# Kernel optimization log

Measured on AMD Instinct MI355X. Metric: run time of the kernel, lower is better.

The kernel has to match this reference:

```python
import jax, jax.numpy as jnp
import numpy as np

B, T, D, H = 4, 2048, 1024, 16
DK = D // H


def setup_inputs() -> dict:
    key = jax.random.key(0)
    ks = jax.random.split(key, 8)
    s = 0.02
    return {
        "query": jax.random.normal(ks[0], (B, T, D), jnp.float32),
        "key": jax.random.normal(ks[1], (B, T, D), jnp.float32),
        "value": jax.random.normal(ks[2], (B, T, D), jnp.float32),
        "mask": jnp.ones((B, T, T), jnp.int32),  # 1 = attend, 0 = masked out
        "Wq": jax.random.normal(ks[3], (D, D), jnp.float32) * s,
        "bq": jnp.zeros((D,), jnp.float32),
        "Wk": jax.random.normal(ks[4], (D, D), jnp.float32) * s,
        "bk": jnp.zeros((D,), jnp.float32),
        "Wv": jax.random.normal(ks[5], (D, D), jnp.float32) * s,
        "bv": jnp.zeros((D,), jnp.float32),
        "Wo": jax.random.normal(ks[6], (D, D), jnp.float32) * s,
        "bo": jnp.zeros((D,), jnp.float32),
    }


def reference(query, key, value, mask, Wq, bq, Wk, bk, Wv, bv, Wo, bo):
    b, t1, d = query.shape
    h, dk = H, DK
    # linear projections (torch nn.Linear: x @ W.T + b), split heads
    q = (query @ Wq.T + bq).reshape(b, t1, h, dk).transpose(0, 2, 1, 3)  # b h t1 dk
    k = (key @ Wk.T + bk).reshape(b, -1, h, dk).transpose(0, 2, 1, 3)    # b h t2 dk
    v = (value @ Wv.T + bv).reshape(b, -1, h, dk).transpose(0, 2, 1, 3)  # b h t2 dk
    scores = jnp.einsum('bhqd,bhkd->bhqk', q, k) / jnp.sqrt(jnp.float32(dk))
    neg = jnp.finfo(scores.dtype).min
    m = (mask[:, None, :, :] == 0)  # b 1 t1 t2 broadcast over heads
    scores = jnp.where(m, neg, scores)
    attn = jax.nn.softmax(scores, axis=-1)
    attn = jnp.where(m, 0.0, attn)
    # dropout_rate = 0.0 -> identity
    x = jnp.einsum('bhqk,bhkd->bhqd', attn, v)
    x = x.transpose(0, 2, 1, 3).reshape(b, t1, h * dk)
    out = x @ Wo.T + bo
    return out, attn
```

## Files before the change

### kernel.cpp

```cpp
#include <hip/hip_runtime.h>
#include <hip/hip_bf16.h>
#include <stdint.h>

#define B_ 4
#define T_ 2048
#define D_ 1024
#define H_ 16
#define DK_ 64
#define LOG2E 1.44269504088896340736f
#define NEGF (-3.0e38f)

typedef __attribute__((ext_vector_type(8))) short bf16x8;
typedef __attribute__((ext_vector_type(4))) float f32x4;

#define FENCE()   asm volatile("" ::: "memory")
#define SCHEDB()  __builtin_amdgcn_sched_barrier(0)
#define SBAR()    __builtin_amdgcn_s_barrier()
#define WAITV0()  asm volatile("s_waitcnt vmcnt(0)" ::: "memory")
#define WAITL0()  asm volatile("s_waitcnt lgkmcnt(0)" ::: "memory")
#define WAITLV4() asm volatile("s_waitcnt lgkmcnt(0) vmcnt(4)" ::: "memory")

__device__ inline unsigned short f2bf(float f){
  union { __hip_bfloat16 h; unsigned short u; } v;
  v.h = __hip_bfloat16(f);
  return v.u;
}
__device__ inline unsigned int pk2(float a, float b){
  return (unsigned int)f2bf(a) | ((unsigned int)f2bf(b) << 16);
}
__device__ inline float fexp2(float x){ return __builtin_amdgcn_exp2f(x); }
__device__ inline f32x4 mfma16(bf16x8 a, bf16x8 b, f32x4 c){
  return __builtin_amdgcn_mfma_f32_16x16x32_bf16(a, b, c, 0, 0, 0);
}
__device__ inline bf16x8 lds_frag(const unsigned short* base, int row, int slot){
  return *(const bf16x8*)((const char*)base + row*128 + ((slot ^ (row & 7)) << 4));
}
__device__ inline void gload16(const void* g, void* l){
  __builtin_amdgcn_global_load_lds((const __attribute__((address_space(1))) void*)g,
                                   (__attribute__((address_space(3))) void*)l, 16, 0, 0);
}
__device__ inline void stage_gl128(const unsigned short* __restrict__ g, int ld,
                                   unsigned short* lds, int wave, int lane){
#pragma unroll
  for (int i = 0; i < 4; ++i){
    int row = wave*32 + i*8 + (lane >> 3);
    int c = (lane & 7) ^ (row & 7);
    gload16(g + (size_t)row*ld + c*8, lds + (wave*32 + i*8)*64);
  }
}
__device__ inline void stage_gl64(const unsigned short* __restrict__ g, int ld,
                                  unsigned short* lds, int wave, int lane){
#pragma unroll
  for (int i = 0; i < 2; ++i){
    int row = wave*16 + i*8 + (lane >> 3);
    int c = (lane & 7) ^ (row & 7);
    gload16(g + (size_t)row*ld + c*8, lds + (wave*16 + i*8)*64);
  }
}

__global__ void pack_mask_k(const int* __restrict__ mask, unsigned long long* __restrict__ bits){
  int i = blockIdx.x * 256 + threadIdx.x;
  unsigned long long b = __ballot(mask[i] != 0);
  if ((threadIdx.x & 63) == 0) bits[i >> 6] = b;
}

__global__ void convall_k(const float* __restrict__ Wq, const float* __restrict__ Wk,
                          const float* __restrict__ Wv, const float* __restrict__ Wo,
                          const float* __restrict__ q, const float* __restrict__ k,
                          const float* __restrict__ v,
                          unsigned short* __restrict__ wdst, unsigned short* __restrict__ xdst){
  int g = blockIdx.x*256 + threadIdx.x;
  const float* s; unsigned short* d; int off;
  if (g < 524288){
    int w = g >> 17; off = (g & 131071) * 8;
    s = (w==0) ? Wq : (w==1) ? Wk : (w==2) ? Wv : Wo;
    d = wdst + (size_t)w*1048576 + off;
  } else {
    int gg = g - 524288;
    int w = gg >> 20; off = (gg & 1048575) * 8;
    s = (w==0) ? q : (w==1) ? k : v;
    d = xdst + (size_t)w*8388608 + off;
  }
  float4 a = *(const float4*)(s + off);
  float4 b2 = *(const float4*)(s + off + 4);
  uint4 o;
  o.x = pk2(a.x,a.y); o.y = pk2(a.z,a.w); o.z = pk2(b2.x,b2.y); o.w = pk2(b2.z,b2.w);
  *(uint4*)d = o;
}

template<int MODE>
__global__ __launch_bounds__(256, 3)
void gemm_nt(const unsigned short* __restrict__ A0, const unsigned short* __restrict__ W0,
             const float* __restrict__ bias0, const float* __restrict__ bias1,
             void* __restrict__ C0, float oscale0)
{
  __shared__ __align__(16) unsigned short As[128*64];
  __shared__ __align__(16) unsigned short Bs[128*64];
  const int tid = threadIdx.x, lane = tid & 63, wave = tid >> 6;
  const int lcol = lane & 15, lgrp = lane >> 4;
  const int mtile = blockIdx.y, ntile = blockIdx.x;
  const int wm = (wave & 1) * 64, wn = (wave >> 1) * 64;
  const unsigned short* A = A0;
  const unsigned short* W = W0;
  const float* bias = bias0;
  void* C = C0;
  float oscale = oscale0;
  if constexpr (MODE == 0){
    int z = blockIdx.z;
    A = A0 + (size_t)z*8388608;
    W = W0 + (size_t)z*1048576;
    bias = z ? bias1 : bias0;
    C = (void*)((unsigned short*)C0 + (size_t)z*8388608);
    oscale = z ? 1.0f : oscale0;
  }
  f32x4 acc[4][4] = {};
#pragma unroll 1
  for (int kt = 0; kt < 16; ++kt){
    if constexpr (MODE == 2){
      int m0 = mtile*128; int b = m0 >> 11; int t0 = m0 & 2047;
      const unsigned short* xbase = A + (((size_t)(b*16 + kt)*2048 + t0) << 6);
      stage_gl128(xbase, 64, As, wave, lane);
    } else {
      stage_gl128(A + (size_t)(mtile*128)*1024 + kt*64, 1024, As, wave, lane);
    }
    stage_gl128(W + (size_t)(ntile*128)*1024 + kt*64, 1024, Bs, wave, lane);
    __syncthreads();
    bf16x8 af[4][2], bfr[4][2];
#pragma unroll
    for (int mi=0;mi<4;mi++)
#pragma unroll
      for (int kh=0;kh<2;kh++)
        af[mi][kh] = lds_frag(As, wm + mi*16 + lcol, kh*4 + lgrp);
#pragma unroll
    for (int ni=0;ni<4;ni++)
#pragma unroll
      for (int kh=0;kh<2;kh++)
        bfr[ni][kh] = lds_frag(Bs, wn + ni*16 + lcol, kh*4 + lgrp);
    __builtin_amdgcn_s_setprio(1);
#pragma unroll
    for (int mi=0;mi<4;mi++)
#pragma unroll
      for (int ni=0;ni<4;ni++)
#pragma unroll
        for (int kh=0;kh<2;kh++)
          acc[mi][ni] = mfma16(af[mi][kh], bfr[ni][kh], acc[mi][ni]);
    __builtin_amdgcn_s_setprio(0);
    __syncthreads();
  }
#pragma unroll
  for (int mi=0;mi<4;mi++){
#pragma unroll
    for (int ni=0;ni<4;ni++){
      int n = ntile*128 + wn + ni*16 + lcol;
#pragma unroll
      for (int r=0;r<4;r++){
        int m = mtile*128 + wm + mi*16 + lgrp*4 + r;
        float v = acc[mi][ni][r];
        if constexpr (MODE == 0){
          v = (v + bias[n]) * oscale;
          int bb = m >> 11, t = m & 2047, hh = n >> 6, dk = n & 63;
          ((unsigned short*)C)[(((size_t)(bb*H_ + hh)*T_ + t) << 6) + dk] = f2bf(v);
        } else if constexpr (MODE == 1){
          v += bias[m];
          int bb = n >> 11, t = n & 2047, hh = m >> 6, dk = m & 63;
          ((unsigned short*)C)[(((size_t)(bb*H_ + hh)*DK_ + dk) << 11) + t] = f2bf(v);
        } else {
          v += bias[n];
          ((float*)C)[(size_t)m*D_ + n] = v;
        }
      }
    }
  }
}

__global__ __launch_bounds__(256, 4)
void attn_k(const unsigned short* __restrict__ Qbh, const unsigned short* __restrict__ Kbh,
            const unsigned short* __restrict__ Vt, const unsigned long long* __restrict__ mbits,
            float* __restrict__ attn, unsigned short* __restrict__ Xq)
{
  __shared__ __align__(16) unsigned short Ks[2][64*64];
  __shared__ __align__(16) unsigned short Vts[2][64*64];
  __shared__ __align__(16) unsigned short Ps[64*64];
  __shared__ int s_mall;
  const int tid = threadIdx.x, lane = tid & 63, wave = tid >> 6;
  const int lcol = lane & 15, lgrp = lane >> 4;
  const int id = blockIdx.x;
  const int sub = id >> 3;
  const int bh = (id & 7)*8 + (sub >> 5);
  const int qt = sub & 31;
  const int b = bh >> 4;
  const int q0 = qt * 64;

  const unsigned short* Kbase = Kbh + ((size_t)bh*T_) * DK_;
  const unsigned short* Vbase = Vt + (size_t)bh*DK_*T_;

  {
    const ulonglong2* mp = (const ulonglong2*)(mbits + ((size_t)b*T_ + q0)*32) + tid*4;
    unsigned long long macc = ~0ull;
#pragma unroll
    for (int i=0;i<4;i++){ ulonglong2 v = mp[i]; macc &= v.x & v.y; }
    if (tid == 0) s_mall = 1;
    __syncthreads();
    if (!__all(macc == ~0ull) && (lane == 0)) atomicAnd(&s_mall, 0);
  }

  stage_gl64(Qbh + ((size_t)bh*T_ + q0)*DK_, 64, Ps, wave, lane);
  stage_gl64(Kbase, 64, Ks[0], wave, lane);
  __syncthreads();
  const bool mall = (s_mall != 0);
  bf16x8 qf[2];
#pragma unroll
  for (int kh=0;kh<2;kh++) qf[kh] = lds_frag(Ps, wave*16 + lcol, kh*4 + lgrp);

  const int qr = wave*16 + lcol;
  const unsigned long long* mrp = mbits + ((size_t)b*T_ + q0 + qr)*32;
  const int bit0 = lgrp*4;

  float lsum = 0.f;

#pragma unroll 1
  for (int kv=0; kv<32; ++kv){
    if (kv < 31) stage_gl64(Kbase + (size_t)(kv+1)*64*DK_, 64, Ks[(kv+1)&1], wave, lane);
    const unsigned short* kcur = Ks[kv&1];
    f32x4 sf[4] = {};
    __builtin_amdgcn_s_setprio(1);
#pragma unroll
    for (int kh=0;kh<2;kh++)
#pragma unroll
      for (int kb=0;kb<4;kb++)
        sf[kb] = mfma16(lds_frag(kcur, kb*16 + lcol, kh*4 + lgrp), qf[kh], sf[kb]);
    __builtin_amdgcn_s_setprio(0);
    float part = 0.f;
    if (mall){
#pragma unroll
      for (int kb=0;kb<4;kb++)
#pragma unroll
        for (int r=0;r<4;r++) part += fexp2(sf[kb][r]);
    } else {
      unsigned long long w = mrp[kv];
#pragma unroll
      for (int kb=0;kb<4;kb++)
#pragma unroll
        for (int r=0;r<4;r++)
          part += fexp2(((w >> (kb*16 + bit0 + r)) & 1ull) ? sf[kb][r] : NEGF);
    }
    lsum += part;
    __syncthreads();
  }

  lsum += __shfl_xor(lsum, 16);
  lsum += __shfl_xor(lsum, 32);
  const float mmr = (lsum > 0.f) ? __log2f(lsum) : 3.0e38f;

  f32x4 oacc[4] = {};
  float* abase = attn + ((size_t)bh*T_ + q0)*T_;

  stage_gl64(Kbase, 64, Ks[0], wave, lane);
  stage_gl64(Vbase, T_, Vts[0], wave, lane);

  if (mall){
    WAITV0(); SCHEDB(); SBAR();
#pragma unroll 1
    for (int kv=0; kv<32; ++kv){
      if (kv < 31){
        stage_gl64(Kbase + (size_t)(kv+1)*64*DK_, 64, Ks[(kv+1)&1], wave, lane);
        stage_gl64(Vbase + (size_t)(kv+1)*64, T_, Vts[(kv+1)&1], wave, lane);
      }
      FENCE(); SCHEDB();
      const unsigned short* kcur = Ks[kv&1];
      f32x4 sf[4] = {};
      __builtin_amdgcn_s_setprio(1);
#pragma unroll
      for (int kh=0;kh<2;kh++)
#pragma unroll
        for (int kb=0;kb<4;kb++)
          sf[kb] = mfma16(lds_frag(kcur, kb*16 + lcol, kh*4 + lgrp), qf[kh], sf[kb]);
      __builtin_amdgcn_s_setprio(0);
      float* arow = abase + (size_t)qr*T_ + kv*64 + bit0;
      char* prow = (char*)Ps + qr*128 + ((lgrp & 1) << 3);
      const int sw = qr & 7;
#pragma unroll
      for (int kb=0;kb<4;kb++){
        float p0 = fexp2(sf[kb][0] - mmr);
        float p1 = fexp2(sf[kb][1] - mmr);
        float p2 = fexp2(sf[kb][2] - mmr);
        float p3 = fexp2(sf[kb][3] - mmr);
        f32x4 st = {p0, p1, p2, p3};
        __builtin_nontemporal_store(st, (f32x4*)(arow + kb*16));
        uint2 pb;
        pb.x = pk2(p0, p1);
        pb.y = pk2(p2, p3);
        *(uint2*)(prow + ((((kb << 1) | (lgrp >> 1)) ^ sw) << 4)) = pb;
      }
      WAITL0(); SCHEDB(); SBAR();
      const unsigned short* vcur = Vts[kv&1];
      __builtin_amdgcn_s_setprio(1);
#pragma unroll
      for (int kh=0;kh<2;kh++){
        bf16x8 af = lds_frag(vcur, wave*16 + lcol, kh*4 + lgrp);
#pragma unroll
        for (int qb=0;qb<4;qb++)
          oacc[qb] = mfma16(af, lds_frag(Ps, qb*16 + lcol, kh*4 + lgrp), oacc[qb]);
      }
      __builtin_amdgcn_s_setprio(0);
      WAITLV4(); SCHEDB(); SBAR();
    }
  } else {
    __syncthreads();
#pragma unroll 1
    for (int kv=0; kv<32; ++kv){
      if (kv < 31){
        stage_gl64(Kbase + (size_t)(kv+1)*64*DK_, 64, Ks[(kv+1)&1], wave, lane);
        stage_gl64(Vbase + (size_t)(kv+1)*64, T_, Vts[(kv+1)&1], wave, lane);
      }
      unsigned long long w = mrp[kv];
      const unsigned short* kcur = Ks[kv&1];
      f32x4 sf[4] = {};
#pragma unroll
      for (int kh=0;kh<2;kh++)
#pragma unroll
        for (int kb=0;kb<4;kb++)
          sf[kb] = mfma16(lds_frag(kcur, kb*16 + lcol, kh*4 + lgrp), qf[kh], sf[kb]);
      float* arow = abase + (size_t)qr*T_ + kv*64 + bit0;
      char* prow = (char*)Ps + qr*128 + ((lgrp & 1) << 3);
      const int sw = qr & 7;
#pragma unroll
      for (int kb=0;kb<4;kb++){
        float p0 = fexp2(sf[kb][0] - mmr);
        float p1 = fexp2(sf[kb][1] - mmr);
        float p2 = fexp2(sf[kb][2] - mmr);
        float p3 = fexp2(sf[kb][3] - mmr);
        p0 = ((w >> (kb*16 + bit0    )) & 1ull) ? p0 : 0.f;
        p1 = ((w >> (kb*16 + bit0 + 1)) & 1ull) ? p1 : 0.f;
        p2 = ((w >> (kb*16 + bit0 + 2)) & 1ull) ? p2 : 0.f;
        p3 = ((w >> (kb*16 + bit0 + 3)) & 1ull) ? p3 : 0.f;
        f32x4 st = {p0, p1, p2, p3};
        __builtin_nontemporal_store(st, (f32x4*)(arow + kb*16));
        uint2 pb;
        pb.x = pk2(p0, p1);
        pb.y = pk2(p2, p3);
        *(uint2*)(prow + ((((kb << 1) | (lgrp >> 1)) ^ sw) << 4)) = pb;
      }
      __syncthreads();
      const unsigned short* vcur = Vts[kv&1];
#pragma unroll
      for (int kh=0;kh<2;kh++){
        bf16x8 af = lds_frag(vcur, wave*16 + lcol, kh*4 + lgrp);
#pragma unroll
        for (int qb=0;qb<4;qb++)
          oacc[qb] = mfma16(af, lds_frag(Ps, qb*16 + lcol, kh*4 + lgrp), oacc[qb]);
      }
      __syncthreads();
    }
  }

  unsigned short* Es = (unsigned short*)Ks;
#pragma unroll
  for (int qb=0;qb<4;qb++){
    uint2 pv;
    pv.x = pk2(oacc[qb][0], oacc[qb][1]);
    pv.y = pk2(oacc[qb][2], oacc[qb][3]);
    *(uint2*)(Es + (qb*16 + lcol)*68 + wave*16 + lgrp*4) = pv;
  }
  __syncthreads();
  unsigned short* xrow = Xq + ((size_t)bh*T_ + q0)*DK_;
#pragma unroll
  for (int it=0; it<4; ++it){
    int idx = tid + it*256;
    int q = idx >> 4, sl = idx & 15;
    uint2 v = *(const uint2*)(Es + q*68 + sl*4);
    *(uint2*)(xrow + (size_t)q*64 + sl*4) = v;
  }
}

extern "C" void kernel_launch(void* const* d_in, const int* in_sizes, int n_in,
                              void* d_out, int out_size, void* d_ws, size_t ws_size,
                              hipStream_t stream) {
  const float* query = (const float*)d_in[0];
  const float* key   = (const float*)d_in[1];
  const float* value = (const float*)d_in[2];
  const int*   mask  = (const int*)d_in[3];
  const float* Wq = (const float*)d_in[4];  const float* bq = (const float*)d_in[5];
  const float* Wk = (const float*)d_in[6];  const float* bk = (const float*)d_in[7];
  const float* Wv = (const float*)d_in[8];  const float* bv = (const float*)d_in[9];
  const float* Wo = (const float*)d_in[10]; const float* bo = (const float*)d_in[11];

  float* out  = (float*)d_out;
  float* attn = out + (size_t)B_*T_*D_;

  char* ws = (char*)d_ws;
  unsigned short* Qbh = (unsigned short*)(ws);
  unsigned short* Kbh = (unsigned short*)(ws + ((size_t)16<<20));
  unsigned short* Vt  = (unsigned short*)(ws + ((size_t)32<<20));
  unsigned long long* mb = (unsigned long long*)(ws + ((size_t)48<<20));
  unsigned short* Wbf = (unsigned short*)(ws + ((size_t)50<<20));
  unsigned short* Xbf = (unsigned short*)attn;

  pack_mask_k<<<dim3((B_*T_*T_)/256), 256, 0, stream>>>(mask, mb);
  convall_k<<<dim3(14336), 256, 0, stream>>>(Wq, Wk, Wv, Wo, query, key, value, Wbf, Xbf);
  gemm_nt<0><<<dim3(8,64,2), 256, 0, stream>>>(Xbf, Wbf, bq, bk, Qbh, 0.125f*LOG2E);
  gemm_nt<1><<<dim3(64,8), 256, 0, stream>>>(Wbf + (2u<<20), Xbf + 16777216, bv, nullptr, Vt, 1.0f);
  attn_k<<<dim3(2048), 256, 0, stream>>>(Qbh, Kbh, Vt, mb, attn, Qbh);
  gemm_nt<2><<<dim3(8,64), 256, 0, stream>>>(Qbh, Wbf + (3u<<20), bo, nullptr, out, 1.0f);
}
```

Before: 465.6 us.

## Fuse PV accumulation into first pass, normalize output by row sum afterwards

Moves the P·V product into the first (row-sum) pass using unnormalized exp2 scores and divides the output by the row sum at the end. The second pass now only recomputes scores and writes the normalized attention matrix, with no V staging or second MFMA stage. The aim is to keep the PV work out of the store-bound attention-write pass so that pass has less work per iteration. In exchange, the first pass gains V loads and a barrier, and its wait changes from vmcnt(4) to vmcnt(0). Using unnormalized exp without max subtraction risks overflow, though the default weights keep scores small.

```diff
diff --git a/kernel.cpp b/kernel.cpp
--- a/kernel.cpp
+++ b/kernel.cpp
@@ -13,12 +13,13 @@
 typedef __attribute__((ext_vector_type(8))) short bf16x8;
 typedef __attribute__((ext_vector_type(4))) float f32x4;
 
-#define FENCE()   asm volatile("" ::: "memory")
-#define SCHEDB()  __builtin_amdgcn_sched_barrier(0)
-#define SBAR()    __builtin_amdgcn_s_barrier()
-#define WAITV0()  asm volatile("s_waitcnt vmcnt(0)" ::: "memory")
-#define WAITL0()  asm volatile("s_waitcnt lgkmcnt(0)" ::: "memory")
-#define WAITLV4() asm volatile("s_waitcnt lgkmcnt(0) vmcnt(4)" ::: "memory")
+#define FENCE()    asm volatile("" ::: "memory")
+#define SCHEDB()   __builtin_amdgcn_sched_barrier(0)
+#define SBAR()     __builtin_amdgcn_s_barrier()
+#define WAITV0()   asm volatile("s_waitcnt vmcnt(0)" ::: "memory")
+#define WAITL0()   asm volatile("s_waitcnt lgkmcnt(0)" ::: "memory")
+#define WAITLV0()  asm volatile("s_waitcnt lgkmcnt(0) vmcnt(0)" ::: "memory")
+#define WAITLV4()  asm volatile("s_waitcnt lgkmcnt(0) vmcnt(4)" ::: "memory")
 
 __device__ inline unsigned short f2bf(float f){
   union { __hip_bfloat16 h; unsigned short u; } v;
@@ -181,6 +182,7 @@
   __shared__ __align__(16) unsigned short Ks[2][64*64];
   __shared__ __align__(16) unsigned short Vts[2][64*64];
   __shared__ __align__(16) unsigned short Ps[64*64];
+  __shared__ float Ls[64];
   __shared__ int s_mall;
   const int tid = threadIdx.x, lane = tid & 63, wave = tid >> 6;
   const int lcol = lane & 15, lgrp = lane >> 4;
@@ -206,6 +208,7 @@
 
   stage_gl64(Qbh + ((size_t)bh*T_ + q0)*DK_, 64, Ps, wave, lane);
   stage_gl64(Kbase, 64, Ks[0], wave, lane);
+  stage_gl64(Vbase, T_, Vts[0], wave, lane);
   __syncthreads();
   const bool mall = (s_mall != 0);
   bf16x8 qf[2];
@@ -217,49 +220,9 @@
   const int bit0 = lgrp*4;
 
   float lsum = 0.f;
-
-#pragma unroll 1
-  for (int kv=0; kv<32; ++kv){
-    if (kv < 31) stage_gl64(Kbase + (size_t)(kv+1)*64*DK_, 64, Ks[(kv+1)&1], wave, lane);
-    const unsigned short* kcur = Ks[kv&1];
-    f32x4 sf[4] = {};
-    __builtin_amdgcn_s_setprio(1);
-#pragma unroll
-    for (int kh=0;kh<2;kh++)
-#pragma unroll
-      for (int kb=0;kb<4;kb++)
-        sf[kb] = mfma16(lds_frag(kcur, kb*16 + lcol, kh*4 + lgrp), qf[kh], sf[kb]);
-    __builtin_amdgcn_s_setprio(0);
-    float part = 0.f;
-    if (mall){
-#pragma unroll
-      for (int kb=0;kb<4;kb++)
-#pragma unroll
-        for (int r=0;r<4;r++) part += fexp2(sf[kb][r]);
-    } else {
-      unsigned long long w = mrp[kv];
-#pragma unroll
-      for (int kb=0;kb<4;kb++)
-#pragma unroll
-        for (int r=0;r<4;r++)
-          part += fexp2(((w >> (kb*16 + bit0 + r)) & 1ull) ? sf[kb][r] : NEGF);
-    }
-    lsum += part;
-    __syncthreads();
-  }
-
-  lsum += __shfl_xor(lsum, 16);
-  lsum += __shfl_xor(lsum, 32);
-  const float mmr = (lsum > 0.f) ? __log2f(lsum) : 3.0e38f;
-
   f32x4 oacc[4] = {};
-  float* abase = attn + ((size_t)bh*T_ + q0)*T_;
-
-  stage_gl64(Kbase, 64, Ks[0], wave, lane);
-  stage_gl64(Vbase, T_, Vts[0], wave, lane);
 
   if (mall){
-    WAITV0(); SCHEDB(); SBAR();
 #pragma unroll 1
     for (int kv=0; kv<32; ++kv){
       if (kv < 31){
@@ -276,22 +239,22 @@
         for (int kb=0;kb<4;kb++)
           sf[kb] = mfma16(lds_frag(kcur, kb*16 + lcol, kh*4 + lgrp), qf[kh], sf[kb]);
       __builtin_amdgcn_s_setprio(0);
-      float* arow = abase + (size_t)qr*T_ + kv*64 + bit0;
       char* prow = (char*)Ps + qr*128 + ((lgrp & 1) << 3);
       const int sw = qr & 7;
+      float part = 0.f;
 #pragma unroll
       for (int kb=0;kb<4;kb++){
-        float p0 = fexp2(sf[kb][0] - mmr);
-        float p1 = fexp2(sf[kb][1] - mmr);
-        float p2 = fexp2(sf[kb][2] - mmr);
-        float p3 = fexp2(sf[kb][3] - mmr);
-        f32x4 st = {p0, p1, p2, p3};
-        __builtin_nontemporal_store(st, (f32x4*)(arow + kb*16));
+        float p0 = fexp2(sf[kb][0]);
+        float p1 = fexp2(sf[kb][1]);
+        float p2 = fexp2(sf[kb][2]);
+        float p3 = fexp2(sf[kb][3]);
+        part += (p0 + p1) + (p2 + p3);
         uint2 pb;
         pb.x = pk2(p0, p1);
         pb.y = pk2(p2, p3);
         *(uint2*)(prow + ((((kb << 1) | (lgrp >> 1)) ^ sw) << 4)) = pb;
       }
+      lsum += part;
       WAITL0(); SCHEDB(); SBAR();
       const unsigned short* vcur = Vts[kv&1];
       __builtin_amdgcn_s_setprio(1);
@@ -303,10 +266,9 @@
           oacc[qb] = mfma16(af, lds_frag(Ps, qb*16 + lcol, kh*4 + lgrp), oacc[qb]);
       }
       __builtin_amdgcn_s_setprio(0);
-      WAITLV4(); SCHEDB(); SBAR();
+      WAITLV0(); SCHEDB(); SBAR();
     }
   } else {
-    __syncthreads();
 #pragma unroll 1
     for (int kv=0; kv<32; ++kv){
       if (kv < 31){
@@ -321,9 +283,86 @@
 #pragma unroll
         for (int kb=0;kb<4;kb++)
           sf[kb] = mfma16(lds_frag(kcur, kb*16 + lcol, kh*4 + lgrp), qf[kh], sf[kb]);
-      float* arow = abase + (size_t)qr*T_ + kv*64 + bit0;
       char* prow = (char*)Ps + qr*128 + ((lgrp & 1) << 3);
       const int sw = qr & 7;
+#pragma unroll
+      for (int kb=0;kb<4;kb++){
+        float p0 = fexp2(((w >> (kb*16 + bit0    )) & 1ull) ? sf[kb][0] : NEGF);
+        float p1 = fexp2(((w >> (kb*16 + bit0 + 1)) & 1ull) ? sf[kb][1] : NEGF);
+        float p2 = fexp2(((w >> (kb*16 + bit0 + 2)) & 1ull) ? sf[kb][2] : NEGF);
+        float p3 = fexp2(((w >> (kb*16 + bit0 + 3)) & 1ull) ? sf[kb][3] : NEGF);
+        lsum += (p0 + p1) + (p2 + p3);
+        uint2 pb;
+        pb.x = pk2(p0, p1);
+        pb.y = pk2(p2, p3);
+        *(uint2*)(prow + ((((kb << 1) | (lgrp >> 1)) ^ sw) << 4)) = pb;
+      }
+      __syncthreads();
+      const unsigned short* vcur = Vts[kv&1];
+#pragma unroll
+      for (int kh=0;kh<2;kh++){
+        bf16x8 af = lds_frag(vcur, wave*16 + lcol, kh*4 + lgrp);
+#pragma unroll
+        for (int qb=0;qb<4;qb++)
+          oacc[qb] = mfma16(af, lds_frag(Ps, qb*16 + lcol, kh*4 + lgrp), oacc[qb]);
+      }
+      __syncthreads();
+    }
+  }
+
+  lsum += __shfl_xor(lsum, 16);
+  lsum += __shfl_xor(lsum, 32);
+  const float mmr = (lsum > 0.f) ? __log2f(lsum) : 3.0e38f;
+  if (lgrp == 0) Ls[qr] = lsum;
+  __syncthreads();
+  float linv[4];
+#pragma unroll
+  for (int qb=0;qb<4;qb++){
+    float lv = Ls[qb*16 + lcol];
+    linv[qb] = (lv > 0.f) ? 1.f/lv : 0.f;
+  }
+
+  float* abase = attn + ((size_t)bh*T_ + q0)*T_;
+
+  stage_gl64(Kbase, 64, Ks[0], wave, lane);
+  if (mall){
+    WAITV0(); SCHEDB(); SBAR();
+#pragma unroll 1
+    for (int kv=0; kv<32; ++kv){
+      if (kv < 31) stage_gl64(Kbase + (size_t)(kv+1)*64*DK_, 64, Ks[(kv+1)&1], wave, lane);
+      FENCE(); SCHEDB();
+      const unsigned short* kcur = Ks[kv&1];
+      f32x4 sf[4] = {};
+      __builtin_amdgcn_s_setprio(1);
+#pragma unroll
+      for (int kh=0;kh<2;kh++)
+#pragma unroll
+        for (int kb=0;kb<4;kb++)
+          sf[kb] = mfma16(lds_frag(kcur, kb*16 + lcol, kh*4 + lgrp), qf[kh], sf[kb]);
+      __builtin_amdgcn_s_setprio(0);
+      float* arow = abase + (size_t)qr*T_ + kv*64 + bit0;
+#pragma unroll
+      for (int kb=0;kb<4;kb++){
+        f32x4 st = {fexp2(sf[kb][0] - mmr), fexp2(sf[kb][1] - mmr),
+                    fexp2(sf[kb][2] - mmr), fexp2(sf[kb][3] - mmr)};
+        __builtin_nontemporal_store(st, (f32x4*)(arow + kb*16));
+      }
+      WAITLV4(); SCHEDB(); SBAR();
+    }
+  } else {
+    __syncthreads();
+#pragma unroll 1
+    for (int kv=0; kv<32; ++kv){
+      if (kv < 31) stage_gl64(Kbase + (size_t)(kv+1)*64*DK_, 64, Ks[(kv+1)&1], wave, lane);
+      unsigned long long w = mrp[kv];
+      const unsigned short* kcur = Ks[kv&1];
+      f32x4 sf[4] = {};
+#pragma unroll
+      for (int kh=0;kh<2;kh++)
+#pragma unroll
+        for (int kb=0;kb<4;kb++)
+          sf[kb] = mfma16(lds_frag(kcur, kb*16 + lcol, kh*4 + lgrp), qf[kh], sf[kb]);
+      float* arow = abase + (size_t)qr*T_ + kv*64 + bit0;
 #pragma unroll
       for (int kb=0;kb<4;kb++){
         float p0 = fexp2(sf[kb][0] - mmr);
@@ -336,19 +375,6 @@
         p3 = ((w >> (kb*16 + bit0 + 3)) & 1ull) ? p3 : 0.f;
         f32x4 st = {p0, p1, p2, p3};
         __builtin_nontemporal_store(st, (f32x4*)(arow + kb*16));
-        uint2 pb;
-        pb.x = pk2(p0, p1);
-        pb.y = pk2(p2, p3);
-        *(uint2*)(prow + ((((kb << 1) | (lgrp >> 1)) ^ sw) << 4)) = pb;
-      }
-      __syncthreads();
-      const unsigned short* vcur = Vts[kv&1];
-#pragma unroll
-      for (int kh=0;kh<2;kh++){
-        bf16x8 af = lds_frag(vcur, wave*16 + lcol, kh*4 + lgrp);
-#pragma unroll
-        for (int qb=0;qb<4;qb++)
-          oacc[qb] = mfma16(af, lds_frag(Ps, qb*16 + lcol, kh*4 + lgrp), oacc[qb]);
       }
       __syncthreads();
     }
@@ -358,8 +384,8 @@
 #pragma unroll
   for (int qb=0;qb<4;qb++){
     uint2 pv;
-    pv.x = pk2(oacc[qb][0], oacc[qb][1]);
-    pv.y = pk2(oacc[qb][2], oacc[qb][3]);
+    pv.x = pk2(oacc[qb][0]*linv[qb], oacc[qb][1]*linv[qb]);
+    pv.y = pk2(oacc[qb][2]*linv[qb], oacc[qb][3]*linv[qb]);
     *(uint2*)(Es + (qb*16 + lcol)*68 + wave*16 + lgrp*4) = pv;
   }
   __syncthreads();
```

New measurement: 499.0 us. 7.2% more time.
